# Performance work log

Measured on AMD Instinct MI355X. Metric: run time of the kernel, lower is better.

Reference implementation:

```python
import jax, jax.numpy as jnp
import numpy as np

NUM_USER = 60000
NUM_ITEM = 40000
DIM = 64
E_U, E_I, E_G = 720000, 480000, 1200000


def _spmm(vals, src, dst, emb, n_rows):
    # sparse.mm(A, emb): out[dst] += A[dst, src] * emb[src]
    return jax.ops.segment_sum(vals[:, None] * emb[src], dst, num_segments=n_rows)


def setup_inputs() -> dict:
    key = jax.random.key(0)
    ks = jax.random.split(key, 11)
    return {
        "users_emb": jax.random.normal(ks[0], (NUM_USER, DIM), dtype=jnp.float32),
        "items_emb": jax.random.normal(ks[1], (NUM_ITEM, DIM), dtype=jnp.float32),
        "user_src": jax.random.randint(ks[2], (E_U,), 0, NUM_USER, dtype=jnp.int32),
        "user_dst": jax.random.randint(ks[3], (E_U,), 0, NUM_USER, dtype=jnp.int32),
        "user_vals": jax.random.uniform(ks[4], (E_U,), dtype=jnp.float32),
        "item_src": jax.random.randint(ks[5], (E_I,), 0, NUM_ITEM, dtype=jnp.int32),
        "item_dst": jax.random.randint(ks[6], (E_I,), 0, NUM_ITEM, dtype=jnp.int32),
        "item_vals": jax.random.uniform(ks[7], (E_I,), dtype=jnp.float32),
        "graph_src": jax.random.randint(ks[8], (E_G,), 0, NUM_USER + NUM_ITEM, dtype=jnp.int32),
        "graph_dst": jax.random.randint(ks[9], (E_G,), 0, NUM_USER + NUM_ITEM, dtype=jnp.int32),
        "graph_vals": jax.random.uniform(ks[10], (E_G,), dtype=jnp.float32),
    }


def reference(users_emb, items_emb, user_src, user_dst, user_vals,
              item_src, item_dst, item_vals, graph_src, graph_dst, graph_vals):
    num_user, num_item = users_emb.shape[0], items_emb.shape[0]
    # h_u1 = sparse.mm(user_mat, users_emb); h_i1 = sparse.mm(item_mat, items_emb)
    h_u1 = _spmm(user_vals, user_src, user_dst, users_emb, num_user)
    h_i1 = _spmm(item_vals, item_src, item_dst, items_emb, num_item)
    # all_emb_tran = sparse.mm(graph, cat([users_emb, items_emb]))  (unused for mode=0)
    all_emb = jnp.concatenate([users_emb, items_emb], axis=0)
    all_tran = _spmm(graph_vals, graph_src, graph_dst, all_emb, num_user + num_item)
    h_u2, h_i2 = all_tran[:num_user], all_tran[num_user:]
    # mode == 0 -> return (h_u1, h_i1)
    return (h_u1, h_i1)
```

## Files before the change

kernel.cpp:

```cpp
#include <hip/hip_runtime.h>
#include <hip/hip_fp16.h>

#define DIM   64
#define TILE  64
#define TSH   6
#define CHUNK 4096
#define ACHUNK 1024
#define CAPMARGIN 256

__global__ void __launch_bounds__(256) spmm_edge_kernel(
    const float* __restrict__ vals, const int* __restrict__ src,
    const int* __restrict__ dst, const float* __restrict__ emb,
    float* __restrict__ out, int n_edges)
{
    int e    = blockIdx.x * 4 + (threadIdx.x >> 6);
    int lane = threadIdx.x & 63;
    if (e >= n_edges) return;
    atomicAdd(&out[(size_t)dst[e] * DIM + lane],
              vals[e] * emb[(size_t)src[e] * DIM + lane]);
}

struct ScatterSM {
    int  lcnt[1024], lscan[1024], gbase[1024], wsum[16];
    int2 stage[CHUNK];
    int  gidx[CHUNK];
};
struct AccumSM {
    int2 stage[ACHUNK];
    int  rs[TILE], rc[TILE];
};
union SMemBig { ScatterSM s; AccumSM a; };

__device__ __forceinline__ void dev_scatter(
    ScatterSM& sm,
    const int* __restrict__ src, const int* __restrict__ dst,
    const float* __restrict__ vals, int n, int base,
    int bucket_base, int cap, int region_base,
    int* __restrict__ bcur, int2* __restrict__ pay)
{
    int tid = threadIdx.x, wid = tid >> 6, lane = tid & 63;
    sm.lcnt[tid] = 0;
    __syncthreads();

    int pk[4], vb[4], bk[4], tk[4]; bool ok[4];
#pragma unroll
    for (int k = 0; k < 4; ++k) {
        int i = base + k * 1024 + tid;
        ok[k] = (i < n);
        if (ok[k]) {
            int s = src[i], d = dst[i];
            vb[k] = __float_as_int(vals[i]);
            bk[k] = d >> TSH;
            pk[k] = (s << TSH) | (d & (TILE - 1));
            tk[k] = atomicAdd(&sm.lcnt[bk[k]], 1);
        }
    }
    __syncthreads();

    int c = sm.lcnt[tid], s = c;
#pragma unroll
    for (int d = 1; d < 64; d <<= 1) {
        int u = __shfl_up(s, d, 64);
        if (lane >= d) s += u;
    }
    if (lane == 63) sm.wsum[wid] = s;
    __syncthreads();
    if (wid == 0 && lane < 16) {
        int v = sm.wsum[lane], t3 = v;
#pragma unroll
        for (int d = 1; d < 16; d <<= 1) {
            int u = __shfl_up(t3, d, 64);
            if (lane >= d) t3 += u;
        }
        sm.wsum[lane] = t3 - v;
    }
    __syncthreads();
    sm.lscan[tid] = s + sm.wsum[wid];
    sm.gbase[tid] = c ? (region_base + tid * cap +
                         atomicAdd(&bcur[bucket_base + tid], c)) : 0;
    __syncthreads();

#pragma unroll
    for (int k = 0; k < 4; ++k)
        if (ok[k]) {
            int b  = bk[k];
            int sp = sm.lscan[b] - sm.lcnt[b] + tk[k];
            sm.stage[sp] = make_int2(pk[k], vb[k]);
            sm.gidx[sp]  = sm.gbase[b] + tk[k];
        }
    __syncthreads();

    int tot = sm.lscan[1023];
    for (int i = tid; i < tot; i += 1024)
        pay[sm.gidx[i]] = sm.stage[i];
}

__device__ __forceinline__ void dev_cvt(
    const float4* __restrict__ in, __half2* __restrict__ dst,
    long n4, int rank, int nblk)
{
    int t = threadIdx.x;
    for (long i = (long)rank * 1024 + t; i < n4; i += (long)nblk * 1024) {
        float4 f = in[i];
        dst[2 * i]     = __floats2half2_rn(f.x, f.y);
        dst[2 * i + 1] = __floats2half2_rn(f.z, f.w);
    }
}

struct H4 { __half2 a, b; };
__device__ __forceinline__ float4 gld4(const __half* e, int rowelem, int gl) {
    H4 h = *((const H4*)(e + rowelem) + gl);
    float2 fa = __half22float2(h.a), fb = __half22float2(h.b);
    return make_float4(fa.x, fa.y, fb.x, fb.y);
}
__device__ __forceinline__ float4 gld4(const float* e, int rowelem, int gl) {
    return *((const float4*)(e + rowelem) + gl);
}

template <typename ET>
__device__ __forceinline__ void dev_accum(
    AccumSM& sm, const int2* __restrict__ pay, int cnt, int start,
    const ET* __restrict__ emb, float* __restrict__ out, int row0, int nrows)
{
    int tid  = threadIdx.x;
    int wid  = tid >> 6;
    int lane = tid & 63;
    int g    = lane >> 4, gl = lane & 15;
    int grp  = wid * 4 + g;

    float4 a = make_float4(0.f, 0.f, 0.f, 0.f);
    int end = start + cnt;

    for (int cb = start; cb < end; cb += ACHUNK) {
        int cn = end - cb; if (cn > ACHUNK) cn = ACHUNK;

        if (tid < TILE) sm.rc[tid] = 0;
        __syncthreads();

        int2 e; int rl = 0, tk = 0; bool ok = (tid < cn);
        if (ok) {
            e  = pay[cb + tid];
            rl = e.x & (TILE - 1);
            tk = atomicAdd(&sm.rc[rl], 1);
        }
        __syncthreads();

        if (wid == 0) {
            int c = sm.rc[lane], s = c;
#pragma unroll
            for (int d = 1; d < 64; d <<= 1) {
                int t = __shfl_up(s, d, 64);
                if (lane >= d) s += t;
            }
            sm.rs[lane] = s - c;
        }
        __syncthreads();

        if (ok) sm.stage[sm.rs[rl] + tk] = e;
        __syncthreads();

        int j = sm.rs[grp], jend = j + sm.rc[grp];
        for (; j + 3 < jend; j += 4) {
            int2 p0 = sm.stage[j], p1 = sm.stage[j + 1],
                 p2 = sm.stage[j + 2], p3 = sm.stage[j + 3];
            float4 g0 = gld4(emb, p0.x & ~(TILE - 1), gl);
            float4 g1 = gld4(emb, p1.x & ~(TILE - 1), gl);
            float4 g2 = gld4(emb, p2.x & ~(TILE - 1), gl);
            float4 g3 = gld4(emb, p3.x & ~(TILE - 1), gl);
            float v0 = __int_as_float(p0.y), v1 = __int_as_float(p1.y);
            float v2 = __int_as_float(p2.y), v3 = __int_as_float(p3.y);
            a.x += v0 * g0.x; a.y += v0 * g0.y; a.z += v0 * g0.z; a.w += v0 * g0.w;
            a.x += v1 * g1.x; a.y += v1 * g1.y; a.z += v1 * g1.z; a.w += v1 * g1.w;
            a.x += v2 * g2.x; a.y += v2 * g2.y; a.z += v2 * g2.z; a.w += v2 * g2.w;
            a.x += v3 * g3.x; a.y += v3 * g3.y; a.z += v3 * g3.z; a.w += v3 * g3.w;
        }
        for (; j < jend; ++j) {
            int2 p = sm.stage[j];
            float4 gg = gld4(emb, p.x & ~(TILE - 1), gl);
            float v = __int_as_float(p.y);
            a.x += v * gg.x; a.y += v * gg.y; a.z += v * gg.z; a.w += v * gg.w;
        }
        __syncthreads();
    }

    int r = row0 + grp;
    if (r < nrows)
        *((float4*)(out + (size_t)r * DIM) + gl) = a;
}

__global__ void __launch_bounds__(1024) phase1_kernel(
    const int* __restrict__ src_u, const int* __restrict__ dst_u,
    const float* __restrict__ val_u, int n_u, int nblk_u,
    int cap_u, int* __restrict__ bcur, int2* __restrict__ pay,
    const float4* __restrict__ cvt_in, __half2* __restrict__ cvt_dst,
    long n4, int nblk_cvt)
{
    __shared__ SMemBig sm;
    if ((int)blockIdx.x < nblk_u)
        dev_scatter(sm.s, src_u, dst_u, val_u, n_u, blockIdx.x * CHUNK,
                    0, cap_u, 0, bcur, pay);
    else
        dev_cvt(cvt_in, cvt_dst, n4, blockIdx.x - nblk_u, nblk_cvt);
}

template <typename ET>
__global__ void __launch_bounds__(1024) phase2_kernel(
    const int* __restrict__ src_i, const int* __restrict__ dst_i,
    const float* __restrict__ val_i, int n_i, int nblk_i,
    int nbu, int cap_u, int cap_i,
    int* __restrict__ bcur, int2* __restrict__ pay,
    const float4* __restrict__ cvt_in, __half2* __restrict__ cvt_dst,
    long n4, int nblk_cvt,
    const ET* __restrict__ emb_u, float* __restrict__ out_u, int nu)
{
    __shared__ SMemBig sm;
    int bx = blockIdx.x;
    if (bx < nblk_i) {
        dev_scatter(sm.s, src_i, dst_i, val_i, n_i, bx * CHUNK,
                    nbu, cap_i, nbu * cap_u, bcur, pay);
    } else if (bx < nblk_i + nblk_cvt) {
        dev_cvt(cvt_in, cvt_dst, n4, bx - nblk_i, nblk_cvt);
    } else {
        int b = bx - nblk_i - nblk_cvt;
        dev_accum<ET>(sm.a, pay, bcur[b], b * cap_u,
                      emb_u, out_u, b << TSH, nu);
    }
}

template <typename ET>
__global__ void __launch_bounds__(1024) phase3_kernel(
    const int2* __restrict__ pay, const int* __restrict__ bcur,
    int nbu, int cap_u, int cap_i,
    const ET* __restrict__ emb_i, float* __restrict__ out_i, int ni)
{
    __shared__ AccumSM sm;
    int b = blockIdx.x;
    dev_accum<ET>(sm, pay, bcur[nbu + b], nbu * cap_u + b * cap_i,
                  emb_i, out_i, b << TSH, ni);
}

extern "C" void kernel_launch(void* const* d_in, const int* in_sizes, int n_in,
                              void* d_out, int out_size, void* d_ws, size_t ws_size,
                              hipStream_t stream)
{
    const float* users_emb = (const float*)d_in[0];
    const float* items_emb = (const float*)d_in[1];
    const int*   user_src  = (const int*)  d_in[2];
    const int*   user_dst  = (const int*)  d_in[3];
    const float* user_vals = (const float*)d_in[4];
    const int*   item_src  = (const int*)  d_in[5];
    const int*   item_dst  = (const int*)  d_in[6];
    const float* item_vals = (const float*)d_in[7];

    const int E_u = in_sizes[2];
    const int E_i = in_sizes[5];
    const int NU  = in_sizes[0] / DIM;
    const int NI  = in_sizes[1] / DIM;

    float* out = (float*)d_out;

    const int NBU = (NU + TILE - 1) / TILE;
    const int NBI = (NI + TILE - 1) / TILE;
    const int NB  = NBU + NBI;

    const int cap_u = (E_u + NBU - 1) / NBU + CAPMARGIN;
    const int cap_i = (E_i + NBI - 1) / NBI + CAPMARGIN;

    size_t hdr_ints    = ((size_t)NB + 1) & ~(size_t)1;
    size_t pay_entries = (size_t)NBU * cap_u + (size_t)NBI * cap_i;
    size_t need_core   = hdr_ints * sizeof(int) + pay_entries * sizeof(int2);
    size_t emb_bytes   = (size_t)(NU + NI) * DIM * sizeof(__half);
    size_t need16      = need_core + emb_bytes;

    if (ws_size < need_core || NU > 65536 || NI > 65536) {
        hipMemsetAsync(d_out, 0, (size_t)out_size * sizeof(float), stream);
        spmm_edge_kernel<<<dim3((E_u + 3) / 4), dim3(256), 0, stream>>>(
            user_vals, user_src, user_dst, users_emb, out, E_u);
        spmm_edge_kernel<<<dim3((E_i + 3) / 4), dim3(256), 0, stream>>>(
            item_vals, item_src, item_dst, items_emb, out + (size_t)NU * DIM, E_i);
        return;
    }

    int*  bcur = (int*)d_ws;
    int2* pay  = (int2*)((int*)d_ws + hdr_ints);

    const bool use_fp16 = (ws_size >= need16);
    __half* embh = (__half*)((char*)d_ws + need_core);

    hipMemsetAsync(bcur, 0, (size_t)NB * sizeof(int), stream);

    const int nblk_u  = (E_u + CHUNK - 1) / CHUNK;
    const int nblk_i  = (E_i + CHUNK - 1) / CHUNK;
    const int cvt_u_b = use_fp16 ? 128 : 0;
    const int cvt_i_b = use_fp16 ? 96  : 0;
    const long n4u    = (long)NU * (DIM / 4);
    const long n4i    = (long)NI * (DIM / 4);

    phase1_kernel<<<dim3(nblk_u + cvt_u_b), dim3(1024), 0, stream>>>(
        user_src, user_dst, user_vals, E_u, nblk_u,
        cap_u, bcur, pay,
        (const float4*)users_emb, (__half2*)embh, n4u, cvt_u_b);

    if (use_fp16) {
        phase2_kernel<__half><<<dim3(nblk_i + cvt_i_b + NBU), dim3(1024), 0, stream>>>(
            item_src, item_dst, item_vals, E_i, nblk_i,
            NBU, cap_u, cap_i, bcur, pay,
            (const float4*)items_emb, (__half2*)(embh + (size_t)NU * DIM), n4i, cvt_i_b,
            embh, out, NU);
        phase3_kernel<__half><<<dim3(NBI), dim3(1024), 0, stream>>>(
            pay, bcur, NBU, cap_u, cap_i,
            embh + (size_t)NU * DIM, out + (size_t)NU * DIM, NI);
    } else {
        phase2_kernel<float><<<dim3(nblk_i + NBU), dim3(1024), 0, stream>>>(
            item_src, item_dst, item_vals, E_i, nblk_i,
            NBU, cap_u, cap_i, bcur, pay,
            (const float4*)items_emb, (__half2*)nullptr, 0, 0,
            users_emb, out, NU);
        phase3_kernel<float><<<dim3(NBI), dim3(1024), 0, stream>>>(
            pay, bcur, NBU, cap_u, cap_i,
            items_emb, out + (size_t)NU * DIM, NI);
    }
}
```

Baseline: 65.56 us.

## Restructure three-phase pipeline into one scatter/convert kernel and one accumulate kernel

Merges the user and item scatter plus both fp16 conversions into a single stage kernel, and moves all accumulation (users and items) into a second kernel. This cuts one kernel launch and gives a simpler two-phase schedule. In exchange it drops the overlap of item scatter with user accumulation. The item-convert block count is also changed slightly.

```diff
diff --git a/kernel.cpp b/kernel.cpp
--- a/kernel.cpp
+++ b/kernel.cpp
@@ -29,7 +29,6 @@
     int2 stage[ACHUNK];
     int  rs[TILE], rc[TILE];
 };
-union SMemBig { ScatterSM s; AccumSM a; };
 
 __device__ __forceinline__ void dev_scatter(
     ScatterSM& sm,
@@ -188,55 +187,49 @@
         *((float4*)(out + (size_t)r * DIM) + gl) = a;
 }
 
-__global__ void __launch_bounds__(1024) phase1_kernel(
+__global__ void __launch_bounds__(1024) stage_kernel(
     const int* __restrict__ src_u, const int* __restrict__ dst_u,
     const float* __restrict__ val_u, int n_u, int nblk_u,
-    int cap_u, int* __restrict__ bcur, int2* __restrict__ pay,
-    const float4* __restrict__ cvt_in, __half2* __restrict__ cvt_dst,
-    long n4, int nblk_cvt)
-{
-    __shared__ SMemBig sm;
-    if ((int)blockIdx.x < nblk_u)
-        dev_scatter(sm.s, src_u, dst_u, val_u, n_u, blockIdx.x * CHUNK,
-                    0, cap_u, 0, bcur, pay);
-    else
-        dev_cvt(cvt_in, cvt_dst, n4, blockIdx.x - nblk_u, nblk_cvt);
-}
-
-template <typename ET>
-__global__ void __launch_bounds__(1024) phase2_kernel(
     const int* __restrict__ src_i, const int* __restrict__ dst_i,
     const float* __restrict__ val_i, int n_i, int nblk_i,
     int nbu, int cap_u, int cap_i,
     int* __restrict__ bcur, int2* __restrict__ pay,
-    const float4* __restrict__ cvt_in, __half2* __restrict__ cvt_dst,
-    long n4, int nblk_cvt,
-    const ET* __restrict__ emb_u, float* __restrict__ out_u, int nu)
-{
-    __shared__ SMemBig sm;
+    const float4* __restrict__ cvtin_u, const float4* __restrict__ cvtin_i,
+    __half2* __restrict__ cvtdst_u, __half2* __restrict__ cvtdst_i,
+    long n4u, long n4i, int cvt_u_b, int cvt_i_b)
+{
+    __shared__ ScatterSM sm;
     int bx = blockIdx.x;
-    if (bx < nblk_i) {
-        dev_scatter(sm.s, src_i, dst_i, val_i, n_i, bx * CHUNK,
+    if (bx < nblk_u) {
+        dev_scatter(sm, src_u, dst_u, val_u, n_u, bx * CHUNK,
+                    0, cap_u, 0, bcur, pay);
+    } else if (bx < nblk_u + nblk_i) {
+        dev_scatter(sm, src_i, dst_i, val_i, n_i, (bx - nblk_u) * CHUNK,
                     nbu, cap_i, nbu * cap_u, bcur, pay);
-    } else if (bx < nblk_i + nblk_cvt) {
-        dev_cvt(cvt_in, cvt_dst, n4, bx - nblk_i, nblk_cvt);
+    } else if (bx < nblk_u + nblk_i + cvt_u_b) {
+        dev_cvt(cvtin_u, cvtdst_u, n4u, bx - nblk_u - nblk_i, cvt_u_b);
     } else {
-        int b = bx - nblk_i - nblk_cvt;
-        dev_accum<ET>(sm.a, pay, bcur[b], b * cap_u,
-                      emb_u, out_u, b << TSH, nu);
+        dev_cvt(cvtin_i, cvtdst_i, n4i, bx - nblk_u - nblk_i - cvt_u_b, cvt_i_b);
     }
 }
 
 template <typename ET>
-__global__ void __launch_bounds__(1024) phase3_kernel(
+__global__ void __launch_bounds__(1024) accum_kernel(
     const int2* __restrict__ pay, const int* __restrict__ bcur,
     int nbu, int cap_u, int cap_i,
-    const ET* __restrict__ emb_i, float* __restrict__ out_i, int ni)
+    const ET* __restrict__ emb_u, const ET* __restrict__ emb_i,
+    float* __restrict__ out_u, float* __restrict__ out_i, int nu, int ni)
 {
     __shared__ AccumSM sm;
     int b = blockIdx.x;
-    dev_accum<ET>(sm, pay, bcur[nbu + b], nbu * cap_u + b * cap_i,
-                  emb_i, out_i, b << TSH, ni);
+    if (b < nbu)
+        dev_accum<ET>(sm, pay, bcur[b], b * cap_u,
+                      emb_u, out_u, b << TSH, nu);
+    else {
+        int bi = b - nbu;
+        dev_accum<ET>(sm, pay, bcur[b], nbu * cap_u + bi * cap_i,
+                      emb_i, out_i, bi << TSH, ni);
+    }
 }
 
 extern "C" void kernel_launch(void* const* d_in, const int* in_sizes, int n_in,
@@ -292,32 +285,27 @@
     const int nblk_u  = (E_u + CHUNK - 1) / CHUNK;
     const int nblk_i  = (E_i + CHUNK - 1) / CHUNK;
     const int cvt_u_b = use_fp16 ? 128 : 0;
-    const int cvt_i_b = use_fp16 ? 96  : 0;
+    const int cvt_i_b = use_fp16 ? 90  : 0;
     const long n4u    = (long)NU * (DIM / 4);
     const long n4i    = (long)NI * (DIM / 4);
 
-    phase1_kernel<<<dim3(nblk_u + cvt_u_b), dim3(1024), 0, stream>>>(
+    stage_kernel<<<dim3(nblk_u + nblk_i + cvt_u_b + cvt_i_b), dim3(1024), 0, stream>>>(
         user_src, user_dst, user_vals, E_u, nblk_u,
-        cap_u, bcur, pay,
-        (const float4*)users_emb, (__half2*)embh, n4u, cvt_u_b);
+        item_src, item_dst, item_vals, E_i, nblk_i,
+        NBU, cap_u, cap_i, bcur, pay,
+        (const float4*)users_emb, (const float4*)items_emb,
+        (__half2*)embh, (__half2*)(embh + (size_t)NU * DIM),
+        n4u, n4i, cvt_u_b, cvt_i_b);
 
     if (use_fp16) {
-        phase2_kernel<__half><<<dim3(nblk_i + cvt_i_b + NBU), dim3(1024), 0, stream>>>(
-            item_src, item_dst, item_vals, E_i, nblk_i,
-            NBU, cap_u, cap_i, bcur, pay,
-            (const float4*)items_emb, (__half2*)(embh + (size_t)NU * DIM), n4i, cvt_i_b,
-            embh, out, NU);
-        phase3_kernel<__half><<<dim3(NBI), dim3(1024), 0, stream>>>(
+        accum_kernel<__half><<<dim3(NB), dim3(1024), 0, stream>>>(
             pay, bcur, NBU, cap_u, cap_i,
-            embh + (size_t)NU * DIM, out + (size_t)NU * DIM, NI);
+            embh, embh + (size_t)NU * DIM,
+            out, out + (size_t)NU * DIM, NU, NI);
     } else {
-        phase2_kernel<float><<<dim3(nblk_i + NBU), dim3(1024), 0, stream>>>(
-            item_src, item_dst, item_vals, E_i, nblk_i,
-            NBU, cap_u, cap_i, bcur, pay,
-            (const float4*)items_emb, (__half2*)nullptr, 0, 0,
-            users_emb, out, NU);
-        phase3_kernel<float><<<dim3(NBI), dim3(1024), 0, stream>>>(
+        accum_kernel<float><<<dim3(NB), dim3(1024), 0, stream>>>(
             pay, bcur, NBU, cap_u, cap_i,
-            items_emb, out + (size_t)NU * DIM, NI);
-    }
-}
+            users_emb, items_emb,
+            out, out + (size_t)NU * DIM, NU, NI);
+    }
+}
```

After: 60.66 us, median of 2. 1.08x faster.
